# Performance work log

Hardware: AMD Instinct MI355X
Metric: run time of the kernel (lower is better)

The kernel has to match this reference:

```python
import jax, jax.numpy as jnp
import numpy as np

K = 1024      # size_codebook
D = 64        # dim_codebook
N = 131072    # number of input vectors
GAMMA = 0.99
ALPHA = 1e-09
BETA = 0.25


def setup_inputs() -> dict:
    key = jax.random.key(0)
    k1, k2, k3 = jax.random.split(key, 3)
    X = jax.random.normal(k1, (N, D), dtype=jnp.float32)
    E = jax.random.normal(k2, (K, D), dtype=jnp.float32)
    cluster_sizes = jnp.zeros((K,), dtype=jnp.float32)
    moving_avg = E  # buffer initialized to a clone of E.weight
    return {"X": X, "E": E, "cluster_sizes": cluster_sizes, "moving_avg": moving_avg}


def reference(X, E, cluster_sizes, moving_avg):
    # squared euclidean distances: [N, K]
    X_sqnorm = jnp.sum(X * X, axis=1, keepdims=True)          # [N, 1]
    E_sqnorm = jnp.sum(E * E, axis=1)[None, :]                # [1, K]
    dist = X_sqnorm + E_sqnorm - 2.0 * (X @ E.T)              # [N, K]
    min_dist = jnp.min(dist, axis=1)                          # [N]
    argmins = jnp.argmin(dist, axis=1)                        # [N]
    Z_embs_raw = E[argmins]                                   # [N, D]

    # commitment loss (codebook is detached in the EMA variant)
    diff = X - jax.lax.stop_gradient(Z_embs_raw)
    loss = BETA * jnp.mean(jnp.sum(diff * diff, axis=1))

    # EMA codebook update (training mode, no-grad in torch)
    counts = jax.ops.segment_sum(jnp.ones((N,), dtype=X.dtype), argmins, num_segments=K)
    cs = GAMMA * cluster_sizes + (1.0 - GAMMA) * counts
    cs = (cs + ALPHA) / (1.0 + ALPHA * K / jnp.sum(cs))
    sums = jax.ops.segment_sum(X, argmins, num_segments=K)    # one_hot.T @ X, [K, D]
    ma = GAMMA * moving_avg + (1.0 - GAMMA) * sums
    E_new = ma / cs[:, None]

    # straight-through estimator
    Z_embs = X + jax.lax.stop_gradient(Z_embs_raw - X)
    return (Z_embs, loss, argmins, min_dist, E_new, cs, ma)
```

## Files before the change

kernel.cpp:

```cpp
#include <hip/hip_runtime.h>
#include <math.h>

#define NN 131072
#define KK 1024
#define DD 64
#define GAMMA 0.99f
#define ALPHA 1e-9f
#define BETA 0.25f

typedef float f32x4 __attribute__((ext_vector_type(4)));
typedef short bf16x8 __attribute__((ext_vector_type(8)));

typedef const __attribute__((address_space(1))) void gv_t;
typedef __attribute__((address_space(3))) void lv_t;

__device__ __constant__ float OMG = (float)(1.0 - 0.99);

__device__ __forceinline__ void split_bf16(float v, unsigned short& h, unsigned short& l) {
    unsigned int b = __float_as_uint(v);
    unsigned int hb = b & 0xFFFF0000u;
    h = (unsigned short)(hb >> 16);
    float r = v - __uint_as_float(hb);
    unsigned int lb = __float_as_uint(r);
    lb += 0x7FFFu + ((lb >> 16) & 1u);
    l = (unsigned short)(lb >> 16);
}

__global__ __launch_bounds__(64)
void vq_prep(const float* __restrict__ E, float4* __restrict__ Efrag,
             float* __restrict__ esqh) {
    int nt = blockIdx.x;
    int l = threadIdx.x;
    int n = nt * 16 + (l & 15);
    int kb = (l >> 4) * 8;
    float ss = 0.f;
    #pragma unroll
    for (int ks = 0; ks < 2; ++ks) {
        const float4* xp = (const float4*)(E + (size_t)n * DD + ks * 32 + kb);
        float4 a = xp[0], b = xp[1];
        float v[8] = {a.x, a.y, a.z, a.w, b.x, b.y, b.z, b.w};
        union { float4 f; unsigned short u[8]; } H, L;
        #pragma unroll
        for (int j = 0; j < 8; ++j) {
            unsigned short hh, ll;
            split_bf16(v[j], hh, ll);
            H.u[j] = hh; L.u[j] = ll;
            ss = fmaf(v[j], v[j], ss);
        }
        int fid = nt * 4 + ks * 2;
        Efrag[(size_t)(fid + 0) * 64 + l] = H.f;
        Efrag[(size_t)(fid + 1) * 64 + l] = L.f;
    }
    ss += __shfl_xor(ss, 16, 64);
    ss += __shfl_xor(ss, 32, 64);
    if (l < 16) esqh[nt * 16 + l] = -0.5f * ss;
}

#define BM 64

__global__ __launch_bounds__(256, 4)
void vq_main(const float* __restrict__ X, const float* __restrict__ E,
             const float4* __restrict__ Efrag, const float* __restrict__ esqh,
             float* __restrict__ argf, float* __restrict__ mind,
             float* __restrict__ Z, int* __restrict__ cursor,
             int* __restrict__ rowlist, float* __restrict__ sumsFB,
             float* __restrict__ loss_part, int cap) {
    __shared__ float4 stg[2][8][64];
    __shared__ float redv[128];
    __shared__ int redi[128];
    __shared__ int bidx[64];
    __shared__ float bsc[64];
    __shared__ float xsqs[64];
    __shared__ int fbflag[64];

    int tid = threadIdx.x;
    int lane = tid & 63, w = tid >> 6;
    int rg = w & 1, cg = w >> 1;
    int lc = lane & 15, lq = lane >> 4;

    size_t bb = (size_t)blockIdx.x * BM;
    size_t R0 = bb + rg * 32;

    int st = (blockIdx.x >> 3) & 31;

    auto stage_tile = [&](float4 (*sb)[64], int nt) {
        int cgs = w >> 1, fp = (w & 1) * 2;
        const float4* gp = Efrag + ((size_t)(cgs * 32 + nt)) * 256 + fp * 64 + lane;
        __builtin_amdgcn_global_load_lds((gv_t*)gp,
                                         (lv_t*)&sb[cgs * 4 + fp][0], 16, 0, 0);
        __builtin_amdgcn_global_load_lds((gv_t*)(gp + 64),
                                         (lv_t*)&sb[cgs * 4 + fp + 1][0], 16, 0, 0);
    };

    stage_tile(stg[0], st);

    bf16x8 ah[2][2], al[2][2];
    #pragma unroll
    for (int mt = 0; mt < 2; ++mt) {
        float xq = 0.f;
        #pragma unroll
        for (int ks = 0; ks < 2; ++ks) {
            const float4* xp =
                (const float4*)(X + (R0 + mt * 16 + lc) * DD + ks * 32 + lq * 8);
            float4 x0 = xp[0], x1 = xp[1];
            float v[8] = {x0.x, x0.y, x0.z, x0.w, x1.x, x1.y, x1.z, x1.w};
            union { bf16x8 s; unsigned short u[8]; } H, L;
            #pragma unroll
            for (int j = 0; j < 8; ++j) {
                unsigned short hh, ll;
                split_bf16(v[j], hh, ll);
                H.u[j] = hh; L.u[j] = ll;
                xq = fmaf(v[j], v[j], xq);
            }
            ah[mt][ks] = H.s;
            al[mt][ks] = L.s;
        }
        xq += __shfl_xor(xq, 16, 64);
        xq += __shfl_xor(xq, 32, 64);
        if (lane < 16) xsqs[rg * 32 + mt * 16 + lane] = xq;
    }

    float bestv[2][4];
    int besti[2][4];
    #pragma unroll
    for (int mt = 0; mt < 2; ++mt)
        #pragma unroll
        for (int r = 0; r < 4; ++r) { bestv[mt][r] = -3.402823466e38f; besti[mt][r] = 0; }

    const float* ep = esqh + cg * 512 + lc;

    auto consume = [&](float4 (*sb)[64], int ntp) {
        float ec = ep[ntp * 16];
        union { float4 f; bf16x8 s; } u0, u1, u2, u3;
        u0.f = sb[cg * 4 + 0][lane];
        u1.f = sb[cg * 4 + 1][lane];
        u2.f = sb[cg * 4 + 2][lane];
        u3.f = sb[cg * 4 + 3][lane];
        f32x4 acc[2];
        #pragma unroll
        for (int mt = 0; mt < 2; ++mt) acc[mt] = (f32x4){ec, ec, ec, ec};
        #pragma unroll
        for (int mt = 0; mt < 2; ++mt)
            acc[mt] = __builtin_amdgcn_mfma_f32_16x16x32_bf16(ah[mt][0], u0.s, acc[mt], 0, 0, 0);
        #pragma unroll
        for (int mt = 0; mt < 2; ++mt)
            acc[mt] = __builtin_amdgcn_mfma_f32_16x16x32_bf16(ah[mt][1], u2.s, acc[mt], 0, 0, 0);
        #pragma unroll
        for (int mt = 0; mt < 2; ++mt)
            acc[mt] = __builtin_amdgcn_mfma_f32_16x16x32_bf16(ah[mt][0], u1.s, acc[mt], 0, 0, 0);
        #pragma unroll
        for (int mt = 0; mt < 2; ++mt)
            acc[mt] = __builtin_amdgcn_mfma_f32_16x16x32_bf16(ah[mt][1], u3.s, acc[mt], 0, 0, 0);
        #pragma unroll
        for (int mt = 0; mt < 2; ++mt)
            acc[mt] = __builtin_amdgcn_mfma_f32_16x16x32_bf16(al[mt][0], u0.s, acc[mt], 0, 0, 0);
        #pragma unroll
        for (int mt = 0; mt < 2; ++mt)
            acc[mt] = __builtin_amdgcn_mfma_f32_16x16x32_bf16(al[mt][1], u2.s, acc[mt], 0, 0, 0);
        int n = cg * 512 + ntp * 16 + lc;
        #pragma unroll
        for (int mt = 0; mt < 2; ++mt)
            #pragma unroll
            for (int r = 0; r < 4; ++r) {
                float sc = acc[mt][r];
                if (sc > bestv[mt][r]) { bestv[mt][r] = sc; besti[mt][r] = n; }
            }
    };

    for (int i = 0; i < 32; i += 2) {
        __syncthreads();
        stage_tile(stg[1], (i + 1 + st) & 31);
        consume(stg[0], (i + st) & 31);
        __syncthreads();
        if (i + 2 < 32) stage_tile(stg[0], (i + 2 + st) & 31);
        consume(stg[1], (i + 1 + st) & 31);
    }

    #pragma unroll
    for (int off = 1; off <= 8; off <<= 1) {
        #pragma unroll
        for (int mt = 0; mt < 2; ++mt) {
            #pragma unroll
            for (int r = 0; r < 4; ++r) {
                float ov = __shfl_xor(bestv[mt][r], off, 64);
                int oi = __shfl_xor(besti[mt][r], off, 64);
                if (ov > bestv[mt][r] || (ov == bestv[mt][r] && oi < besti[mt][r])) {
                    bestv[mt][r] = ov; besti[mt][r] = oi;
                }
            }
        }
    }
    if (lc == 0) {
        #pragma unroll
        for (int mt = 0; mt < 2; ++mt)
            #pragma unroll
            for (int r = 0; r < 4; ++r) {
                int row = rg * 32 + mt * 16 + lq * 4 + r;
                redv[row * 2 + cg] = bestv[mt][r];
                redi[row * 2 + cg] = besti[mt][r];
            }
    }
    __syncthreads();
    if (tid < 64) {
        float v0 = redv[tid * 2], v1 = redv[tid * 2 + 1];
        int i0 = redi[tid * 2], i1 = redi[tid * 2 + 1];
        int pick = (v1 > v0 || (v1 == v0 && i1 < i0));
        bidx[tid] = pick ? i1 : i0;
        bsc[tid] = pick ? v1 : v0;
    }
    __syncthreads();

    if (tid < 64) {
        int row = tid;
        int bi = bidx[row];
        size_t grow = bb + row;
        float md = fmaf(-2.f, bsc[row], xsqs[row]);
        mind[grow] = md;
        argf[grow] = (float)bi;
        int pos = atomicAdd(&cursor[bi], 1);
        if (pos < cap) {
            rowlist[(size_t)bi * cap + pos] = (int)grow;
            fbflag[row] = 0;
        } else {
            fbflag[row] = 1;
        }
        #pragma unroll
        for (int m = 32; m; m >>= 1) md += __shfl_xor(md, m, 64);
        if (tid == 0) atomicAdd(&loss_part[blockIdx.x & 1023], md);
    }
    __syncthreads();

    #pragma unroll 4
    for (int it = 0; it < 16; ++it) {
        int row = w * 16 + it;
        int bi = bidx[row];
        size_t grow = bb + row;
        float e = E[(size_t)bi * DD + lane];
        Z[grow * DD + lane] = e;
        if (fbflag[row]) {
            float x = X[grow * DD + lane];
            atomicAdd(&sumsFB[(size_t)bi * DD + lane], x);
        }
    }
}

__global__ __launch_bounds__(1024)
void vq_sum_ema(const float* __restrict__ X, const int* __restrict__ rowlist,
                const int* __restrict__ cursor, const float* __restrict__ sumsFB,
                const float* __restrict__ cluster_sizes,
                const float* __restrict__ loss_part, const float* __restrict__ mavg,
                float* __restrict__ o_ma, float* __restrict__ o_enew,
                float* __restrict__ o_cs, float* __restrict__ o_loss, int cap) {
    __shared__ float part[16][64];
    __shared__ float redt[16];
    int k = blockIdx.x;
    int lane = threadIdx.x & 63, w = threadIdx.x >> 6;

    float t = GAMMA * cluster_sizes[threadIdx.x] + OMG * (float)cursor[threadIdx.x];
    #pragma unroll
    for (int m = 32; m; m >>= 1) t += __shfl_xor(t, m, 64);
    if (lane == 0) redt[w] = t;
    __syncthreads();
    float total = 0.f;
    #pragma unroll
    for (int j = 0; j < 16; ++j) total += redt[j];

    float csr = GAMMA * cluster_sizes[k] + OMG * (float)cursor[k];
    float cs = (csr + ALPHA) / (1.0f + (ALPHA * (float)KK) / total);
    if (threadIdx.x == 0) o_cs[k] = cs;

    if (k == 0) {
        __syncthreads();
        float t2 = loss_part[threadIdx.x];
        #pragma unroll
        for (int m = 32; m; m >>= 1) t2 += __shfl_xor(t2, m, 64);
        if (lane == 0) redt[w] = t2;
        __syncthreads();
        if (threadIdx.x == 0) {
            float l = 0.f;
            #pragma unroll
            for (int j = 0; j < 16; ++j) l += redt[j];
            o_loss[0] = BETA * (l / (float)NN);
        }
    }

    int cnt = cursor[k];
    int nr = cnt < cap ? cnt : cap;
    const int* rl = rowlist + (size_t)k * cap;
    float acc = 0.f;
    #pragma unroll 4
    for (int i = w; i < nr; i += 16) {
        int r = rl[i];
        acc += X[(size_t)r * DD + lane];
    }
    part[w][lane] = acc;
    __syncthreads();
    if (w == 0) {
        float s = sumsFB[(size_t)k * DD + lane];
        #pragma unroll
        for (int j = 0; j < 16; ++j) s += part[j][lane];
        float ma = GAMMA * mavg[(size_t)k * DD + lane] + OMG * s;
        o_ma[(size_t)k * DD + lane] = ma;
        o_enew[(size_t)k * DD + lane] = ma / cs;
    }
}

extern "C" void kernel_launch(void* const* d_in, const int* in_sizes, int n_in,
                              void* d_out, int out_size, void* d_ws, size_t ws_size,
                              hipStream_t stream) {
    const float* X = (const float*)d_in[0];
    const float* E = (const float*)d_in[1];
    const float* cluster_sizes = (const float*)d_in[2];
    const float* moving_avg = (const float*)d_in[3];

    float* out = (float*)d_out;
    float* o_Z = out;
    float* o_loss = o_Z + (size_t)NN * DD;
    float* o_arg = o_loss + 1;
    float* o_mind = o_arg + NN;
    float* o_enew = o_mind + NN;
    float* o_cs = o_enew + (size_t)KK * DD;
    float* o_ma = o_cs + KK;

    int* cursor = (int*)d_ws;
    float* loss_part = (float*)d_ws + 1024;
    float* sumsFB = loss_part + 1024;
    float* esqh = sumsFB + (size_t)KK * DD;
    float4* Efrag = (float4*)(esqh + KK);
    int* rowlist = (int*)(esqh + KK + (size_t)KK * DD);

    size_t base_bytes = (size_t)(1024 + 1024 + KK * DD + KK + KK * DD) * 4;
    long cap_l = ((long)ws_size - (long)base_bytes) / (long)(KK * sizeof(int));
    int cap = cap_l < 0 ? 0 : (cap_l > 1024 ? 1024 : (int)cap_l);

    hipMemsetAsync(d_ws, 0, (size_t)(1024 + 1024 + KK * DD) * 4, stream);

    vq_prep<<<KK / 16, 64, 0, stream>>>(E, Efrag, esqh);
    vq_main<<<NN / BM, 256, 0, stream>>>(X, E, Efrag, esqh, o_arg, o_mind, o_Z,
                                         cursor, rowlist, sumsFB, loss_part, cap);
    vq_sum_ema<<<KK, 1024, 0, stream>>>(X, rowlist, cursor, sumsFB, cluster_sizes,
                                        loss_part, moving_avg, o_ma, o_enew,
                                        o_cs, o_loss, cap);
}
```

Measured before the change: 202.8 us.

## Fuse prep, main and EMA kernels into one cooperative persistent kernel

Replaces the memset plus three kernel launches with a single cooperative kernel of 512 persistent blocks. Grid-wide syncs separate the phases: codebook split and workspace zeroing, then the distance/argmin loop over row tiles, then the per-cluster sum and EMA update. The goal is to remove launch and memset overhead and the tail gaps between kernels. In exchange it pays two grid barriers, and the EMA phase now has only 256 threads per cluster instead of 1024, which may slow the gather.

```diff
diff --git a/kernel.cpp b/kernel.cpp
--- a/kernel.cpp
+++ b/kernel.cpp
@@ -1,5 +1,8 @@
 #include <hip/hip_runtime.h>
+#include <hip/hip_cooperative_groups.h>
 #include <math.h>
+
+namespace cg = cooperative_groups;
 
 #define NN 131072
 #define KK 1024
@@ -7,6 +10,10 @@
 #define GAMMA 0.99f
 #define ALPHA 1e-9f
 #define BETA 0.25f
+
+#define BM 64
+#define NTILES (NN / BM)
+#define GRID 512
 
 typedef float f32x4 __attribute__((ext_vector_type(4)));
 typedef short bf16x8 __attribute__((ext_vector_type(8)));
@@ -26,45 +33,20 @@
     l = (unsigned short)(lb >> 16);
 }
 
-__global__ __launch_bounds__(64)
-void vq_prep(const float* __restrict__ E, float4* __restrict__ Efrag,
-             float* __restrict__ esqh) {
-    int nt = blockIdx.x;
-    int l = threadIdx.x;
-    int n = nt * 16 + (l & 15);
-    int kb = (l >> 4) * 8;
-    float ss = 0.f;
-    #pragma unroll
-    for (int ks = 0; ks < 2; ++ks) {
-        const float4* xp = (const float4*)(E + (size_t)n * DD + ks * 32 + kb);
-        float4 a = xp[0], b = xp[1];
-        float v[8] = {a.x, a.y, a.z, a.w, b.x, b.y, b.z, b.w};
-        union { float4 f; unsigned short u[8]; } H, L;
-        #pragma unroll
-        for (int j = 0; j < 8; ++j) {
-            unsigned short hh, ll;
-            split_bf16(v[j], hh, ll);
-            H.u[j] = hh; L.u[j] = ll;
-            ss = fmaf(v[j], v[j], ss);
-        }
-        int fid = nt * 4 + ks * 2;
-        Efrag[(size_t)(fid + 0) * 64 + l] = H.f;
-        Efrag[(size_t)(fid + 1) * 64 + l] = L.f;
-    }
-    ss += __shfl_xor(ss, 16, 64);
-    ss += __shfl_xor(ss, 32, 64);
-    if (l < 16) esqh[nt * 16 + l] = -0.5f * ss;
-}
-
-#define BM 64
+#define WSZERO (1024 + 1024 + KK * DD)
 
 __global__ __launch_bounds__(256, 4)
-void vq_main(const float* __restrict__ X, const float* __restrict__ E,
-             const float4* __restrict__ Efrag, const float* __restrict__ esqh,
-             float* __restrict__ argf, float* __restrict__ mind,
-             float* __restrict__ Z, int* __restrict__ cursor,
-             int* __restrict__ rowlist, float* __restrict__ sumsFB,
-             float* __restrict__ loss_part, int cap) {
+void vq_fused(const float* __restrict__ X, const float* __restrict__ E,
+              float4* __restrict__ Efrag, float* __restrict__ esqh,
+              float* __restrict__ argf, float* __restrict__ mind,
+              float* __restrict__ Z, int* __restrict__ cursor,
+              int* __restrict__ rowlist, float* __restrict__ sumsFB,
+              float* __restrict__ loss_part,
+              const float* __restrict__ cluster_sizes,
+              const float* __restrict__ mavg,
+              float* __restrict__ o_ma, float* __restrict__ o_enew,
+              float* __restrict__ o_cs, float* __restrict__ o_loss,
+              float4* __restrict__ wsz4, int cap) {
     __shared__ float4 stg[2][8][64];
     __shared__ float redv[128];
     __shared__ int redi[128];
@@ -72,236 +54,267 @@
     __shared__ float bsc[64];
     __shared__ float xsqs[64];
     __shared__ int fbflag[64];
+    __shared__ float part[4][64];
+    __shared__ float redt[4];
 
     int tid = threadIdx.x;
     int lane = tid & 63, w = tid >> 6;
-    int rg = w & 1, cg = w >> 1;
+    int rg = w & 1, cgv = w >> 1;
     int lc = lane & 15, lq = lane >> 4;
-
-    size_t bb = (size_t)blockIdx.x * BM;
-    size_t R0 = bb + rg * 32;
-
-    int st = (blockIdx.x >> 3) & 31;
-
-    auto stage_tile = [&](float4 (*sb)[64], int nt) {
-        int cgs = w >> 1, fp = (w & 1) * 2;
-        const float4* gp = Efrag + ((size_t)(cgs * 32 + nt)) * 256 + fp * 64 + lane;
-        __builtin_amdgcn_global_load_lds((gv_t*)gp,
-                                         (lv_t*)&sb[cgs * 4 + fp][0], 16, 0, 0);
-        __builtin_amdgcn_global_load_lds((gv_t*)(gp + 64),
-                                         (lv_t*)&sb[cgs * 4 + fp + 1][0], 16, 0, 0);
-    };
-
-    stage_tile(stg[0], st);
-
-    bf16x8 ah[2][2], al[2][2];
-    #pragma unroll
-    for (int mt = 0; mt < 2; ++mt) {
-        float xq = 0.f;
+    int bid = blockIdx.x;
+
+    if (bid < 16) {
+        int nt = bid * 4 + w;
+        int n = nt * 16 + lc;
+        int kb = lq * 8;
+        float ss = 0.f;
         #pragma unroll
         for (int ks = 0; ks < 2; ++ks) {
-            const float4* xp =
-                (const float4*)(X + (R0 + mt * 16 + lc) * DD + ks * 32 + lq * 8);
-            float4 x0 = xp[0], x1 = xp[1];
-            float v[8] = {x0.x, x0.y, x0.z, x0.w, x1.x, x1.y, x1.z, x1.w};
-            union { bf16x8 s; unsigned short u[8]; } H, L;
+            const float4* xp = (const float4*)(E + (size_t)n * DD + ks * 32 + kb);
+            float4 a = xp[0], b = xp[1];
+            float v[8] = {a.x, a.y, a.z, a.w, b.x, b.y, b.z, b.w};
+            union { float4 f; unsigned short u[8]; } H, L;
             #pragma unroll
             for (int j = 0; j < 8; ++j) {
                 unsigned short hh, ll;
                 split_bf16(v[j], hh, ll);
                 H.u[j] = hh; L.u[j] = ll;
-                xq = fmaf(v[j], v[j], xq);
-            }
-            ah[mt][ks] = H.s;
-            al[mt][ks] = L.s;
-        }
-        xq += __shfl_xor(xq, 16, 64);
-        xq += __shfl_xor(xq, 32, 64);
-        if (lane < 16) xsqs[rg * 32 + mt * 16 + lane] = xq;
-    }
-
-    float bestv[2][4];
-    int besti[2][4];
+                ss = fmaf(v[j], v[j], ss);
+            }
+            int fid = nt * 4 + ks * 2;
+            Efrag[(size_t)(fid + 0) * 64 + lane] = H.f;
+            Efrag[(size_t)(fid + 1) * 64 + lane] = L.f;
+        }
+        ss += __shfl_xor(ss, 16, 64);
+        ss += __shfl_xor(ss, 32, 64);
+        if (lane < 16) esqh[nt * 16 + lane] = -0.5f * ss;
+    } else {
+        int gid = (bid - 16) * 256 + tid;
+        for (int i = gid; i < WSZERO / 4; i += (GRID - 16) * 256)
+            wsz4[i] = (float4){0.f, 0.f, 0.f, 0.f};
+    }
+    __threadfence();
+    cg::this_grid().sync();
+
+    for (int tile = bid; tile < NTILES; tile += GRID) {
+        __syncthreads();
+
+        size_t bb = (size_t)tile * BM;
+        size_t R0 = bb + rg * 32;
+        int st = (tile >> 3) & 31;
+
+        auto stage_tile = [&](float4 (*sb)[64], int nt) {
+            int cgs = w >> 1, fp = (w & 1) * 2;
+            const float4* gp =
+                Efrag + ((size_t)(cgs * 32 + nt)) * 256 + fp * 64 + lane;
+            __builtin_amdgcn_global_load_lds((gv_t*)gp,
+                                             (lv_t*)&sb[cgs * 4 + fp][0], 16, 0, 0);
+            __builtin_amdgcn_global_load_lds((gv_t*)(gp + 64),
+                                             (lv_t*)&sb[cgs * 4 + fp + 1][0], 16, 0, 0);
+        };
+
+        stage_tile(stg[0], st);
+
+        bf16x8 ah[2][2], al[2][2];
+        #pragma unroll
+        for (int mt = 0; mt < 2; ++mt) {
+            float xq = 0.f;
+            #pragma unroll
+            for (int ks = 0; ks < 2; ++ks) {
+                const float4* xp =
+                    (const float4*)(X + (R0 + mt * 16 + lc) * DD + ks * 32 + lq * 8);
+                float4 x0 = xp[0], x1 = xp[1];
+                float v[8] = {x0.x, x0.y, x0.z, x0.w, x1.x, x1.y, x1.z, x1.w};
+                union { bf16x8 s; unsigned short u[8]; } H, L;
+                #pragma unroll
+                for (int j = 0; j < 8; ++j) {
+                    unsigned short hh, ll;
+                    split_bf16(v[j], hh, ll);
+                    H.u[j] = hh; L.u[j] = ll;
+                    xq = fmaf(v[j], v[j], xq);
+                }
+                ah[mt][ks] = H.s;
+                al[mt][ks] = L.s;
+            }
+            xq += __shfl_xor(xq, 16, 64);
+            xq += __shfl_xor(xq, 32, 64);
+            if (lane < 16) xsqs[rg * 32 + mt * 16 + lane] = xq;
+        }
+
+        float bestv[2][4];
+        int besti[2][4];
+        #pragma unroll
+        for (int mt = 0; mt < 2; ++mt)
+            #pragma unroll
+            for (int r = 0; r < 4; ++r) { bestv[mt][r] = -3.402823466e38f; besti[mt][r] = 0; }
+
+        const float* ep = esqh + cgv * 512 + lc;
+
+        auto consume = [&](float4 (*sb)[64], int ntp) {
+            float ec = ep[ntp * 16];
+            union { float4 f; bf16x8 s; } u0, u1, u2, u3;
+            u0.f = sb[cgv * 4 + 0][lane];
+            u1.f = sb[cgv * 4 + 1][lane];
+            u2.f = sb[cgv * 4 + 2][lane];
+            u3.f = sb[cgv * 4 + 3][lane];
+            f32x4 acc[2];
+            #pragma unroll
+            for (int mt = 0; mt < 2; ++mt) acc[mt] = (f32x4){ec, ec, ec, ec};
+            #pragma unroll
+            for (int mt = 0; mt < 2; ++mt)
+                acc[mt] = __builtin_amdgcn_mfma_f32_16x16x32_bf16(ah[mt][0], u0.s, acc[mt], 0, 0, 0);
+            #pragma unroll
+            for (int mt = 0; mt < 2; ++mt)
+                acc[mt] = __builtin_amdgcn_mfma_f32_16x16x32_bf16(ah[mt][1], u2.s, acc[mt], 0, 0, 0);
+            #pragma unroll
+            for (int mt = 0; mt < 2; ++mt)
+                acc[mt] = __builtin_amdgcn_mfma_f32_16x16x32_bf16(ah[mt][0], u1.s, acc[mt], 0, 0, 0);
+            #pragma unroll
+            for (int mt = 0; mt < 2; ++mt)
+                acc[mt] = __builtin_amdgcn_mfma_f32_16x16x32_bf16(ah[mt][1], u3.s, acc[mt], 0, 0, 0);
+            #pragma unroll
+            for (int mt = 0; mt < 2; ++mt)
+                acc[mt] = __builtin_amdgcn_mfma_f32_16x16x32_bf16(al[mt][0], u0.s, acc[mt], 0, 0, 0);
+            #pragma unroll
+            for (int mt = 0; mt < 2; ++mt)
+                acc[mt] = __builtin_amdgcn_mfma_f32_16x16x32_bf16(al[mt][1], u2.s, acc[mt], 0, 0, 0);
+            int n = cgv * 512 + ntp * 16 + lc;
+            #pragma unroll
+            for (int mt = 0; mt < 2; ++mt)
+                #pragma unroll
+                for (int r = 0; r < 4; ++r) {
+                    float sc = acc[mt][r];
+                    if (sc > bestv[mt][r]) { bestv[mt][r] = sc; besti[mt][r] = n; }
+                }
+        };
+
+        for (int i = 0; i < 32; i += 2) {
+            __syncthreads();
+            stage_tile(stg[1], (i + 1 + st) & 31);
+            consume(stg[0], (i + st) & 31);
+            __syncthreads();
+            if (i + 2 < 32) stage_tile(stg[0], (i + 2 + st) & 31);
+            consume(stg[1], (i + 1 + st) & 31);
+        }
+
+        #pragma unroll
+        for (int off = 1; off <= 8; off <<= 1) {
+            #pragma unroll
+            for (int mt = 0; mt < 2; ++mt) {
+                #pragma unroll
+                for (int r = 0; r < 4; ++r) {
+                    float ov = __shfl_xor(bestv[mt][r], off, 64);
+                    int oi = __shfl_xor(besti[mt][r], off, 64);
+                    if (ov > bestv[mt][r] || (ov == bestv[mt][r] && oi < besti[mt][r])) {
+                        bestv[mt][r] = ov; besti[mt][r] = oi;
+                    }
+                }
+            }
+        }
+        if (lc == 0) {
+            #pragma unroll
+            for (int mt = 0; mt < 2; ++mt)
+                #pragma unroll
+                for (int r = 0; r < 4; ++r) {
+                    int row = rg * 32 + mt * 16 + lq * 4 + r;
+                    redv[row * 2 + cgv] = bestv[mt][r];
+                    redi[row * 2 + cgv] = besti[mt][r];
+                }
+        }
+        __syncthreads();
+        if (tid < 64) {
+            float v0 = redv[tid * 2], v1 = redv[tid * 2 + 1];
+            int i0 = redi[tid * 2], i1 = redi[tid * 2 + 1];
+            int pick = (v1 > v0 || (v1 == v0 && i1 < i0));
+            bidx[tid] = pick ? i1 : i0;
+            bsc[tid] = pick ? v1 : v0;
+        }
+        __syncthreads();
+
+        if (tid < 64) {
+            int row = tid;
+            int bi = bidx[row];
+            size_t grow = bb + row;
+            float md = fmaf(-2.f, bsc[row], xsqs[row]);
+            mind[grow] = md;
+            argf[grow] = (float)bi;
+            int pos = atomicAdd(&cursor[bi], 1);
+            if (pos < cap) {
+                rowlist[(size_t)bi * cap + pos] = (int)grow;
+                fbflag[row] = 0;
+            } else {
+                fbflag[row] = 1;
+            }
+            #pragma unroll
+            for (int m = 32; m; m >>= 1) md += __shfl_xor(md, m, 64);
+            if (tid == 0) atomicAdd(&loss_part[tile & 1023], md);
+        }
+        __syncthreads();
+
+        #pragma unroll 4
+        for (int it = 0; it < 16; ++it) {
+            int row = w * 16 + it;
+            int bi = bidx[row];
+            size_t grow = bb + row;
+            float e = E[(size_t)bi * DD + lane];
+            Z[grow * DD + lane] = e;
+            if (fbflag[row]) {
+                float x = X[grow * DD + lane];
+                atomicAdd(&sumsFB[(size_t)bi * DD + lane], x);
+            }
+        }
+    }
+    __threadfence();
+    cg::this_grid().sync();
+
+    float t = 0.f;
     #pragma unroll
-    for (int mt = 0; mt < 2; ++mt)
-        #pragma unroll
-        for (int r = 0; r < 4; ++r) { bestv[mt][r] = -3.402823466e38f; besti[mt][r] = 0; }
-
-    const float* ep = esqh + cg * 512 + lc;
-
-    auto consume = [&](float4 (*sb)[64], int ntp) {
-        float ec = ep[ntp * 16];
-        union { float4 f; bf16x8 s; } u0, u1, u2, u3;
-        u0.f = sb[cg * 4 + 0][lane];
-        u1.f = sb[cg * 4 + 1][lane];
-        u2.f = sb[cg * 4 + 2][lane];
-        u3.f = sb[cg * 4 + 3][lane];
-        f32x4 acc[2];
-        #pragma unroll
-        for (int mt = 0; mt < 2; ++mt) acc[mt] = (f32x4){ec, ec, ec, ec};
-        #pragma unroll
-        for (int mt = 0; mt < 2; ++mt)
-            acc[mt] = __builtin_amdgcn_mfma_f32_16x16x32_bf16(ah[mt][0], u0.s, acc[mt], 0, 0, 0);
-        #pragma unroll
-        for (int mt = 0; mt < 2; ++mt)
-            acc[mt] = __builtin_amdgcn_mfma_f32_16x16x32_bf16(ah[mt][1], u2.s, acc[mt], 0, 0, 0);
-        #pragma unroll
-        for (int mt = 0; mt < 2; ++mt)
-            acc[mt] = __builtin_amdgcn_mfma_f32_16x16x32_bf16(ah[mt][0], u1.s, acc[mt], 0, 0, 0);
-        #pragma unroll
-        for (int mt = 0; mt < 2; ++mt)
-            acc[mt] = __builtin_amdgcn_mfma_f32_16x16x32_bf16(ah[mt][1], u3.s, acc[mt], 0, 0, 0);
-        #pragma unroll
-        for (int mt = 0; mt < 2; ++mt)
-            acc[mt] = __builtin_amdgcn_mfma_f32_16x16x32_bf16(al[mt][0], u0.s, acc[mt], 0, 0, 0);
-        #pragma unroll
-        for (int mt = 0; mt < 2; ++mt)
-            acc[mt] = __builtin_amdgcn_mfma_f32_16x16x32_bf16(al[mt][1], u2.s, acc[mt], 0, 0, 0);
-        int n = cg * 512 + ntp * 16 + lc;
-        #pragma unroll
-        for (int mt = 0; mt < 2; ++mt)
-            #pragma unroll
-            for (int r = 0; r < 4; ++r) {
-                float sc = acc[mt][r];
-                if (sc > bestv[mt][r]) { bestv[mt][r] = sc; besti[mt][r] = n; }
-            }
-    };
-
-    for (int i = 0; i < 32; i += 2) {
-        __syncthreads();
-        stage_tile(stg[1], (i + 1 + st) & 31);
-        consume(stg[0], (i + st) & 31);
-        __syncthreads();
-        if (i + 2 < 32) stage_tile(stg[0], (i + 2 + st) & 31);
-        consume(stg[1], (i + 1 + st) & 31);
-    }
-
-    #pragma unroll
-    for (int off = 1; off <= 8; off <<= 1) {
-        #pragma unroll
-        for (int mt = 0; mt < 2; ++mt) {
-            #pragma unroll
-            for (int r = 0; r < 4; ++r) {
-                float ov = __shfl_xor(bestv[mt][r], off, 64);
-                int oi = __shfl_xor(besti[mt][r], off, 64);
-                if (ov > bestv[mt][r] || (ov == bestv[mt][r] && oi < besti[mt][r])) {
-                    bestv[mt][r] = ov; besti[mt][r] = oi;
-                }
-            }
-        }
-    }
-    if (lc == 0) {
-        #pragma unroll
-        for (int mt = 0; mt < 2; ++mt)
-            #pragma unroll
-            for (int r = 0; r < 4; ++r) {
-                int row = rg * 32 + mt * 16 + lq * 4 + r;
-                redv[row * 2 + cg] = bestv[mt][r];
-                redi[row * 2 + cg] = besti[mt][r];
-            }
-    }
-    __syncthreads();
-    if (tid < 64) {
-        float v0 = redv[tid * 2], v1 = redv[tid * 2 + 1];
-        int i0 = redi[tid * 2], i1 = redi[tid * 2 + 1];
-        int pick = (v1 > v0 || (v1 == v0 && i1 < i0));
-        bidx[tid] = pick ? i1 : i0;
-        bsc[tid] = pick ? v1 : v0;
-    }
-    __syncthreads();
-
-    if (tid < 64) {
-        int row = tid;
-        int bi = bidx[row];
-        size_t grow = bb + row;
-        float md = fmaf(-2.f, bsc[row], xsqs[row]);
-        mind[grow] = md;
-        argf[grow] = (float)bi;
-        int pos = atomicAdd(&cursor[bi], 1);
-        if (pos < cap) {
-            rowlist[(size_t)bi * cap + pos] = (int)grow;
-            fbflag[row] = 0;
-        } else {
-            fbflag[row] = 1;
-        }
-        #pragma unroll
-        for (int m = 32; m; m >>= 1) md += __shfl_xor(md, m, 64);
-        if (tid == 0) atomicAdd(&loss_part[blockIdx.x & 1023], md);
-    }
-    __syncthreads();
-
-    #pragma unroll 4
-    for (int it = 0; it < 16; ++it) {
-        int row = w * 16 + it;
-        int bi = bidx[row];
-        size_t grow = bb + row;
-        float e = E[(size_t)bi * DD + lane];
-        Z[grow * DD + lane] = e;
-        if (fbflag[row]) {
-            float x = X[grow * DD + lane];
-            atomicAdd(&sumsFB[(size_t)bi * DD + lane], x);
-        }
-    }
-}
-
-__global__ __launch_bounds__(1024)
-void vq_sum_ema(const float* __restrict__ X, const int* __restrict__ rowlist,
-                const int* __restrict__ cursor, const float* __restrict__ sumsFB,
-                const float* __restrict__ cluster_sizes,
-                const float* __restrict__ loss_part, const float* __restrict__ mavg,
-                float* __restrict__ o_ma, float* __restrict__ o_enew,
-                float* __restrict__ o_cs, float* __restrict__ o_loss, int cap) {
-    __shared__ float part[16][64];
-    __shared__ float redt[16];
-    int k = blockIdx.x;
-    int lane = threadIdx.x & 63, w = threadIdx.x >> 6;
-
-    float t = GAMMA * cluster_sizes[threadIdx.x] + OMG * (float)cursor[threadIdx.x];
+    for (int j = 0; j < 4; ++j) {
+        int c = tid + j * 256;
+        t += GAMMA * cluster_sizes[c] + OMG * (float)cursor[c];
+    }
     #pragma unroll
     for (int m = 32; m; m >>= 1) t += __shfl_xor(t, m, 64);
     if (lane == 0) redt[w] = t;
     __syncthreads();
-    float total = 0.f;
-    #pragma unroll
-    for (int j = 0; j < 16; ++j) total += redt[j];
-
-    float csr = GAMMA * cluster_sizes[k] + OMG * (float)cursor[k];
-    float cs = (csr + ALPHA) / (1.0f + (ALPHA * (float)KK) / total);
-    if (threadIdx.x == 0) o_cs[k] = cs;
-
-    if (k == 0) {
-        __syncthreads();
-        float t2 = loss_part[threadIdx.x];
-        #pragma unroll
-        for (int m = 32; m; m >>= 1) t2 += __shfl_xor(t2, m, 64);
-        if (lane == 0) redt[w] = t2;
-        __syncthreads();
-        if (threadIdx.x == 0) {
-            float l = 0.f;
-            #pragma unroll
-            for (int j = 0; j < 16; ++j) l += redt[j];
-            o_loss[0] = BETA * (l / (float)NN);
-        }
-    }
-
-    int cnt = cursor[k];
-    int nr = cnt < cap ? cnt : cap;
-    const int* rl = rowlist + (size_t)k * cap;
-    float acc = 0.f;
-    #pragma unroll 4
-    for (int i = w; i < nr; i += 16) {
-        int r = rl[i];
-        acc += X[(size_t)r * DD + lane];
-    }
-    part[w][lane] = acc;
+    float total = redt[0] + redt[1] + redt[2] + redt[3];
     __syncthreads();
-    if (w == 0) {
-        float s = sumsFB[(size_t)k * DD + lane];
-        #pragma unroll
-        for (int j = 0; j < 16; ++j) s += part[j][lane];
-        float ma = GAMMA * mavg[(size_t)k * DD + lane] + OMG * s;
-        o_ma[(size_t)k * DD + lane] = ma;
-        o_enew[(size_t)k * DD + lane] = ma / cs;
+
+    if (bid == 0) {
+        float l2 = 0.f;
+        #pragma unroll
+        for (int j = 0; j < 4; ++j) l2 += loss_part[tid + j * 256];
+        #pragma unroll
+        for (int m = 32; m; m >>= 1) l2 += __shfl_xor(l2, m, 64);
+        if (lane == 0) redt[w] = l2;
+    }
+    __syncthreads();
+    if (bid == 0 && tid == 0)
+        o_loss[0] = BETA * ((redt[0] + redt[1] + redt[2] + redt[3]) / (float)NN);
+
+    for (int k2 = 0; k2 < 2; ++k2) {
+        int k = bid * 2 + k2;
+        __syncthreads();
+        int cnt = cursor[k];
+        int nr = cnt < cap ? cnt : cap;
+        const int* rl = rowlist + (size_t)k * cap;
+        float acc = 0.f;
+        #pragma unroll 4
+        for (int i = w; i < nr; i += 4)
+            acc += X[(size_t)rl[i] * DD + lane];
+        part[w][lane] = acc;
+        __syncthreads();
+        if (w == 0) {
+            float s = sumsFB[(size_t)k * DD + lane];
+            #pragma unroll
+            for (int j = 0; j < 4; ++j) s += part[j][lane];
+            float csr = GAMMA * cluster_sizes[k] + OMG * (float)cursor[k];
+            float cs = (csr + ALPHA) / (1.0f + (ALPHA * (float)KK) / total);
+            float ma = GAMMA * mavg[(size_t)k * DD + lane] + OMG * s;
+            o_ma[(size_t)k * DD + lane] = ma;
+            o_enew[(size_t)k * DD + lane] = ma / cs;
+            if (lane == 0) o_cs[k] = cs;
+        }
     }
 }
 
@@ -328,17 +341,19 @@
     float* esqh = sumsFB + (size_t)KK * DD;
     float4* Efrag = (float4*)(esqh + KK);
     int* rowlist = (int*)(esqh + KK + (size_t)KK * DD);
+    float4* wsz4 = (float4*)d_ws;
 
     size_t base_bytes = (size_t)(1024 + 1024 + KK * DD + KK + KK * DD) * 4;
     long cap_l = ((long)ws_size - (long)base_bytes) / (long)(KK * sizeof(int));
     int cap = cap_l < 0 ? 0 : (cap_l > 1024 ? 1024 : (int)cap_l);
 
-    hipMemsetAsync(d_ws, 0, (size_t)(1024 + 1024 + KK * DD) * 4, stream);
-
-    vq_prep<<<KK / 16, 64, 0, stream>>>(E, Efrag, esqh);
-    vq_main<<<NN / BM, 256, 0, stream>>>(X, E, Efrag, esqh, o_arg, o_mind, o_Z,
-                                         cursor, rowlist, sumsFB, loss_part, cap);
-    vq_sum_ema<<<KK, 1024, 0, stream>>>(X, rowlist, cursor, sumsFB, cluster_sizes,
-                                        loss_part, moving_avg, o_ma, o_enew,
-                                        o_cs, o_loss, cap);
+    void* args[] = {(void*)&X, (void*)&E, (void*)&Efrag, (void*)&esqh,
+                    (void*)&o_arg, (void*)&o_mind, (void*)&o_Z, (void*)&cursor,
+                    (void*)&rowlist, (void*)&sumsFB, (void*)&loss_part,
+                    (void*)&cluster_sizes, (void*)&moving_avg, (void*)&o_ma,
+                    (void*)&o_enew, (void*)&o_cs, (void*)&o_loss,
+                    (void*)&wsz4, (void*)&cap};
+
+    hipLaunchCooperativeKernel((const void*)vq_fused, dim3(GRID), dim3(256),
+                               args, 0, stream);
 }
```

New measurement: 427.2 us. 2.11x slower.
